# Performance work log

Measured on AMD Instinct MI355X. Metric: run time of the kernel, lower is better.

Reference implementation:

```python
import jax, jax.numpy as jnp
import numpy as np

EPS = 1e-5

def _layernorm(x, g, b):
    mu = jnp.mean(x, axis=-1, keepdims=True)
    var = jnp.mean((x - mu) ** 2, axis=-1, keepdims=True)
    return (x - mu) * jax.lax.rsqrt(var + EPS) * g + b

def setup_inputs() -> dict:
    key = jax.random.key(0)
    ks = jax.random.split(key, 16)
    B, C, H, W = 2, 64, 96, 96
    HID = 256
    s = 0.02
    inp = {
        "x": jax.random.normal(ks[0], (B, C, H, W), dtype=jnp.float32),
        "mask": jax.random.randint(ks[1], (B, H, W), 0, 2, dtype=jnp.int32),
        "wq": jax.random.normal(ks[2], (C, C), dtype=jnp.float32) * s,
        "bq": jnp.zeros((C,), dtype=jnp.float32),
        "wk": jax.random.normal(ks[3], (C, C), dtype=jnp.float32) * s,
        "bk": jnp.zeros((C,), dtype=jnp.float32),
        "wv": jax.random.normal(ks[4], (C, C), dtype=jnp.float32) * s,
        "bv": jnp.zeros((C,), dtype=jnp.float32),
        "wo": jax.random.normal(ks[5], (C, C), dtype=jnp.float32) * s,
        "bo": jnp.zeros((C,), dtype=jnp.float32),
        "g1": jnp.ones((C,), dtype=jnp.float32),
        "b1": jnp.zeros((C,), dtype=jnp.float32),
        "g2": jnp.ones((C,), dtype=jnp.float32),
        "b2": jnp.zeros((C,), dtype=jnp.float32),
        "w1": jax.random.normal(ks[6], (HID, C), dtype=jnp.float32) * s,
        "bf1": jnp.zeros((HID,), dtype=jnp.float32),
        "w2": jax.random.normal(ks[7], (C, HID), dtype=jnp.float32) * s,
        "bf2": jnp.zeros((C,), dtype=jnp.float32),
    }
    return inp

def reference(x, mask, wq, bq, wk, bk, wv, bv, wo, bo, g1, b1, g2, b2, w1, bf1, w2, bf2):
    B, C, H, W = x.shape
    scale = C ** (-0.5)
    xf = jnp.transpose(x, (0, 2, 3, 1)).reshape(B, H * W, C)   # [B,N,C]
    m = mask.reshape(B, H * W).astype(bool)                     # [B,N] valid pillars
    # pre-norm (original norms the gathered valid feats; LN is per-token so dense is equivalent)
    h = _layernorm(xf, g1, b1)
    q = h @ wq.T + bq
    k = h @ wk.T + bk
    v = h @ wv.T + bv
    scores = jnp.einsum('bnc,bmc->bnm', q, k) * scale
    scores = jnp.where(m[:, None, :], scores, -1e9)            # attend only among valid keys
    attn = jax.nn.softmax(scores, axis=-1)
    att = jnp.einsum('bnm,bmc->bnc', attn, v)
    h2 = h + (att @ wo.T + bo)                                  # residual onto norm1 output (as in source)
    h2 = _layernorm(h2, g2, b2)
    out = h2 + (jax.nn.gelu(h2 @ w1.T + bf1, approximate=False) @ w2.T + bf2)
    out = jnp.where(m[:, :, None], out, 0.0)                    # scatter-back: invalid positions are zeros
    return jnp.transpose(out.reshape(B, H, W, C), (0, 3, 1, 2))
```

## Files before the change

kernel.cpp:

```cpp
#include <hip/hip_runtime.h>

#define HW     9216
#define NTOK   18432
#define SPLITS 8
#define KIT    (HW / SPLITS / 32)

typedef float  floatx4 __attribute__((ext_vector_type(4)));
typedef short  short8  __attribute__((ext_vector_type(8)));
typedef short  short4v __attribute__((ext_vector_type(4)));
typedef int    int4v   __attribute__((ext_vector_type(4)));

#if __has_builtin(__builtin_amdgcn_exp2f)
#define EXP2F(x) __builtin_amdgcn_exp2f(x)
#else
#define EXP2F(x) exp2f(x)
#endif

__device__ __forceinline__ unsigned short f2bf(float f) {
  unsigned int u = __float_as_uint(f);
  u += 0x7fffu + ((u >> 16) & 1u);
  return (unsigned short)(u >> 16);
}
__device__ __forceinline__ float bf2f(unsigned short s) {
  return __uint_as_float(((unsigned int)s) << 16);
}
__device__ __forceinline__ int pk2(float a, float b) {
  unsigned ua = __float_as_uint(a) + 0x8000u;
  unsigned ub = __float_as_uint(b) + 0x8000u;
  return (int)((ua >> 16) | (ub & 0xffff0000u));
}

__global__ __launch_bounds__(256) void k_qkv(
    const float* __restrict__ x,
    const float* __restrict__ wq, const float* __restrict__ bq,
    const float* __restrict__ wk, const float* __restrict__ bk,
    const float* __restrict__ wv, const float* __restrict__ bv,
    const float* __restrict__ g1, const float* __restrict__ b1,
    const int* __restrict__ mask,
    const float* __restrict__ wo, const float* __restrict__ w1,
    const float* __restrict__ w2,
    unsigned short* __restrict__ h_bf, unsigned short* __restrict__ qg,
    unsigned short* __restrict__ ksw, unsigned short* __restrict__ vsw,
    float* __restrict__ maskf, unsigned short* __restrict__ wobf,
    unsigned short* __restrict__ w1bf, unsigned short* __restrict__ w2bf,
    float* __restrict__ cntb)
{
  __shared__ __align__(16) char usmem[27648];
  float (*xt)[33] = (float (*)[33])usmem;
  unsigned short (*wb)[64][72] = (unsigned short (*)[64][72])usmem;

  __shared__ unsigned short hq[32][72];
  __shared__ unsigned short kt[32][72];
  __shared__ unsigned short vt[64][40];
  __shared__ unsigned short qt[32][72];
  __shared__ float mk32[32];

  const int tid = threadIdx.x, wid = tid >> 6, c = tid & 63;
  const int mcol = c & 15, quad = c >> 4;
  const int bx = blockIdx.x;
  const int t0 = bx * 32;
  const int b  = t0 / HW, n0 = t0 % HW;

  if (tid < 32) {
    const float m = mask[t0 + tid] ? 1.f : 0.f;
    maskf[t0 + tid] = m;
    mk32[tid] = m;
  }
  if (wid == 0) {
    const bool mm = (c < 32) ? (mask[t0 + c] == 0) : false;
    const unsigned long long bal = __ballot(mm);
    if (c == 0) cntb[bx] = (float)__popcll(bal);
  }
  if (bx < 16)       { const int i = bx * 256 + tid;        wobf[i] = f2bf(wo[i]); }
  else if (bx < 80)  { const int i = (bx - 16) * 256 + tid; w1bf[i] = f2bf(w1[i]); }
  else if (bx < 144) { const int i = (bx - 80) * 256 + tid; w2bf[i] = f2bf(w2[i]); }

  #pragma unroll
  for (int p = 0; p < 2; ++p) {
    const int idx = p * 256 + tid;
    const int cc = idx >> 3, t4 = (idx & 7) * 4;
    const floatx4 v = *(const floatx4*)(x + ((long)b * 64 + cc) * HW + n0 + t4);
    xt[cc][t4 + 0] = v[0]; xt[cc][t4 + 1] = v[1];
    xt[cc][t4 + 2] = v[2]; xt[cc][t4 + 3] = v[3];
  }
  __syncthreads();

  {
    const float g1v = g1[c], b1v = b1[c];
    #pragma unroll
    for (int tt = 0; tt < 8; ++tt) {
      const int tok = wid * 8 + tt;
      const float val = xt[c][tok];
      float s = val, q = val * val;
      #pragma unroll
      for (int d = 1; d < 64; d <<= 1) { s += __shfl_xor(s, d); q += __shfl_xor(q, d); }
      const float mu  = s * (1.f / 64.f);
      const float var = q * (1.f / 64.f) - mu * mu;
      const float hv  = (val - mu) * rsqrtf(var + 1e-5f) * g1v + b1v;
      hq[tok][c] = f2bf(hv);
    }
  }
  __syncthreads();

  {
    const int tok = tid >> 3, c8 = (tid & 7) * 8;
    *(short8*)(h_bf + (long)(t0 + tok) * 64 + c8) = *(const short8*)(&hq[tok][c8]);
  }

  {
    auto conv = [&](const float* __restrict__ W, int mwi) {
      #pragma unroll
      for (int j = 0; j < 4; ++j) {
        const int idx4 = (j * 256 + tid) * 4;
        const int o = idx4 >> 6, in4 = idx4 & 63;
        const floatx4 w4 = *(const floatx4*)(W + idx4);
        short4v s4;
        s4[0] = (short)f2bf(w4[0]); s4[1] = (short)f2bf(w4[1]);
        s4[2] = (short)f2bf(w4[2]); s4[3] = (short)f2bf(w4[3]);
        *(short4v*)(&wb[mwi][o][in4]) = s4;
      }
    };
    conv(wq, 0); conv(wk, 1); conv(wv, 2);
  }
  __syncthreads();

  {
    const float QSC = 0.125f * 1.44269504088896f;
    #pragma unroll
    for (int i = 0; i < 6; ++i) {
      const int t = wid * 6 + i;
      const int mat  = t >> 3;
      const int tokT = (t >> 2) & 1;
      const int outT = t & 3;
      const int out  = outT * 16 + mcol;
      const short8 A0 = *(const short8*)(&hq[tokT * 16 + mcol][quad * 8]);
      const short8 A1 = *(const short8*)(&hq[tokT * 16 + mcol][32 + quad * 8]);
      const short8 B0 = *(const short8*)(&wb[mat][out][quad * 8]);
      const short8 B1 = *(const short8*)(&wb[mat][out][32 + quad * 8]);
      floatx4 d = (floatx4){0.f, 0.f, 0.f, 0.f};
      d = __builtin_amdgcn_mfma_f32_16x16x32_bf16(A0, B0, d, 0, 0, 0);
      d = __builtin_amdgcn_mfma_f32_16x16x32_bf16(A1, B1, d, 0, 0, 0);
      if (mat == 0) {
        const float bias = bq[out];
        #pragma unroll
        for (int r = 0; r < 4; ++r) {
          const int tok = tokT * 16 + quad * 4 + r;
          qt[tok][out] = f2bf((d[r] + bias) * QSC);
        }
      } else if (mat == 1) {
        const float bias = bk[out];
        #pragma unroll
        for (int r = 0; r < 4; ++r) {
          const int tok = tokT * 16 + quad * 4 + r;
          kt[tok][out] = f2bf((d[r] + bias) * mk32[tok]);
        }
      } else {
        const float bias = bv[out];
        #pragma unroll
        for (int r = 0; r < 4; ++r) {
          const int tok = tokT * 16 + quad * 4 + r;
          vt[out][tok] = f2bf((d[r] + bias) * mk32[tok]);
        }
      }
    }
  }
  __syncthreads();

  {
    const int tok = tid >> 3, c8 = (tid & 7) * 8;
    *(short8*)(qg + (long)(t0 + tok) * 64 + c8) = *(const short8*)(&qt[tok][c8]);
  }

  const long tile = (long)b * 288 + (n0 >> 5);
  {
    const int slot = tid >> 6, l = tid & 63;
    const int m = l & 15, qd = l >> 4, sub = slot >> 1, ss = slot & 1;
    const short8 v8 = *(const short8*)(&kt[sub * 16 + m][ss * 32 + qd * 8]);
    *(short8*)(ksw + tile * 2048 + tid * 8) = v8;
  }
  {
    const int f = tid >> 6, l = tid & 63;
    const int m = l & 15, qd = l >> 4;
    const short4v lo = *(const short4v*)(&vt[f * 16 + m][qd * 4]);
    const short4v hi = *(const short4v*)(&vt[f * 16 + m][16 + qd * 4]);
    short8 v8;
    v8[0] = lo[0]; v8[1] = lo[1]; v8[2] = lo[2]; v8[3] = lo[3];
    v8[4] = hi[0]; v8[5] = hi[1]; v8[6] = hi[2]; v8[7] = hi[3];
    *(short8*)(vsw + tile * 2048 + tid * 8) = v8;
  }
}

__global__ __launch_bounds__(256, 4) void k_attn(
    const unsigned short* __restrict__ qg, const unsigned short* __restrict__ ksw,
    const unsigned short* __restrict__ vsw,
    unsigned short* __restrict__ opart, float* __restrict__ lpart)
{
  __shared__ __align__(16) char smem[17408];

  const int tid = threadIdx.x, wid = tid >> 6, lane = tid & 63;
  const int mcol = lane & 15, quad = lane >> 4;
  const int bx = blockIdx.x;
  const int split = bx & (SPLITS - 1), qidx = bx / SPLITS;
  const int b = qidx / 48, qt = qidx % 48;
  const long t0q = (long)b * HW + qt * 192 + wid * 48;

  const unsigned short* kswt = ksw + ((long)b * 288 + split * KIT) * 2048;
  const unsigned short* vswt = vsw + ((long)b * 288 + split * KIT) * 2048;

  short8 qf[3][2];
  #pragma unroll
  for (int g = 0; g < 3; ++g)
    #pragma unroll
    for (int s = 0; s < 2; ++s)
      qf[g][s] = *(const short8*)(qg + (t0q + g * 16 + mcol) * 64 + s * 32 + quad * 8);

  short8 ones8;
  #pragma unroll
  for (int i = 0; i < 8; ++i) ones8[i] = (short)0x3F80;

  floatx4 oT[3][4], oL[3];
  #pragma unroll
  for (int g = 0; g < 3; ++g) {
    #pragma unroll
    for (int f = 0; f < 4; ++f) oT[g][f] = (floatx4){0.f,0.f,0.f,0.f};
    oL[g] = (floatx4){0.f,0.f,0.f,0.f};
  }

  short8 kr = *(const short8*)(kswt + tid * 8);
  short8 vr = *(const short8*)(vswt + tid * 8);
  *(short8*)((unsigned short*)smem + tid * 8) = kr;
  *(short8*)((unsigned short*)(smem + 4096) + tid * 8) = vr;
  __syncthreads();

  for (int it = 0; it < KIT; ++it) {
    const int off = (it & 1) * 8192;
    const unsigned short* kfc = (const unsigned short*)(smem + off);
    const unsigned short* vfc = (const unsigned short*)(smem + off + 4096);
    if (it + 1 < KIT) {
      kr = *(const short8*)(kswt + (it + 1) * 2048 + tid * 8);
      vr = *(const short8*)(vswt + (it + 1) * 2048 + tid * 8);
    }

    const short8 kA00 = *(const short8*)(kfc + (0 * 64 + lane) * 8);
    const short8 kA01 = *(const short8*)(kfc + (1 * 64 + lane) * 8);
    const short8 kA10 = *(const short8*)(kfc + (2 * 64 + lane) * 8);
    const short8 kA11 = *(const short8*)(kfc + (3 * 64 + lane) * 8);

    short8 pf[3];
    #pragma unroll
    for (int g = 0; g < 3; ++g) {
      floatx4 s0 = (floatx4){0.f,0.f,0.f,0.f}, s1 = (floatx4){0.f,0.f,0.f,0.f};
      s0 = __builtin_amdgcn_mfma_f32_16x16x32_bf16(kA00, qf[g][0], s0, 0, 0, 0);
      s0 = __builtin_amdgcn_mfma_f32_16x16x32_bf16(kA01, qf[g][1], s0, 0, 0, 0);
      s1 = __builtin_amdgcn_mfma_f32_16x16x32_bf16(kA10, qf[g][0], s1, 0, 0, 0);
      s1 = __builtin_amdgcn_mfma_f32_16x16x32_bf16(kA11, qf[g][1], s1, 0, 0, 0);

      int4v pv;
      pv[0] = pk2(EXP2F(s0[0]), EXP2F(s0[1]));
      pv[1] = pk2(EXP2F(s0[2]), EXP2F(s0[3]));
      pv[2] = pk2(EXP2F(s1[0]), EXP2F(s1[1]));
      pv[3] = pk2(EXP2F(s1[2]), EXP2F(s1[3]));
      pf[g] = __builtin_bit_cast(short8, pv);
      oL[g] = __builtin_amdgcn_mfma_f32_16x16x32_bf16(ones8, pf[g], oL[g], 0, 0, 0);
    }

    #pragma unroll
    for (int f = 0; f < 4; ++f) {
      const short8 vA = *(const short8*)(vfc + (f * 64 + lane) * 8);
      #pragma unroll
      for (int g = 0; g < 3; ++g)
        oT[g][f] = __builtin_amdgcn_mfma_f32_16x16x32_bf16(vA, pf[g], oT[g][f], 0, 0, 0);
    }

    if (it + 1 < KIT) {
      unsigned short* kfn = (unsigned short*)(smem + (off ^ 8192));
      unsigned short* vfn = (unsigned short*)(smem + (off ^ 8192) + 4096);
      *(short8*)(kfn + tid * 8) = kr;
      *(short8*)(vfn + tid * 8) = vr;
    }
    __syncthreads();
  }

  float* scr = (float*)smem + wid * 1088;
  #pragma unroll
  for (int g = 0; g < 3; ++g) {
    #pragma unroll
    for (int f = 0; f < 4; ++f)
      #pragma unroll
      for (int r = 0; r < 4; ++r)
        scr[(quad * 4 + r) * 68 + f * 16 + mcol] = oT[g][f][r];
    #pragma unroll
    for (int ps = 0; ps < 2; ++ps) {
      const int row = ps * 8 + (lane >> 3), cb = (lane & 7) * 8;
      const floatx4 a = *(const floatx4*)(scr + row * 68 + cb);
      const floatx4 c = *(const floatx4*)(scr + row * 68 + cb + 4);
      int4v pk;
      pk[0] = pk2(a[0], a[1]); pk[1] = pk2(a[2], a[3]);
      pk[2] = pk2(c[0], c[1]); pk[3] = pk2(c[2], c[3]);
      *(int4v*)(opart + ((long)split * NTOK + t0q + g * 16 + row) * 64 + cb) = pk;
    }
  }
  if (lane < 16) {
    #pragma unroll
    for (int g = 0; g < 3; ++g)
      lpart[(long)split * NTOK + t0q + g * 16 + lane] = oL[g][0];
  }
}

__global__ __launch_bounds__(256) void k_post(
    const unsigned short* __restrict__ opart, const float* __restrict__ lpart,
    const unsigned short* __restrict__ h_bf, const float* __restrict__ maskf,
    const float* __restrict__ cntb,
    const unsigned short* __restrict__ wobf, const float* __restrict__ bo,
    const float* __restrict__ g2, const float* __restrict__ b2,
    const unsigned short* __restrict__ w1bf, const float* __restrict__ bf1,
    const unsigned short* __restrict__ w2bf, const float* __restrict__ bf2,
    float* __restrict__ out)
{
  __shared__ float          h2_lds[32 * 68];
  __shared__ unsigned short att_lds[32 * 72];
  __shared__ unsigned short hn_lds[32 * 72];
  __shared__ unsigned short g_lds[32 * 264];
  __shared__ float          ot_lds[32 * 68];
  __shared__ float          linv[32];
  __shared__ float          st_mu[32], st_rs[32];
  __shared__ float          nred[4];

  const int tid = threadIdx.x, wid = tid >> 6, lane = tid & 63;
  const int mcol = lane & 15, quad = lane >> 4;
  const int t0 = blockIdx.x * 32;
  const int b = t0 / HW, n0 = t0 % HW;

  {
    float cacc = 0.f;
    for (int i = tid; i < 288; i += 256) cacc += cntb[b * 288 + i];
    #pragma unroll
    for (int d = 1; d < 64; d <<= 1) cacc += __shfl_xor(cacc, d);
    if (lane == 0) nred[wid] = cacc;
  }

  const int tok = tid >> 3, c8 = (tid & 7) * 8;
  float o[8];
  #pragma unroll
  for (int i = 0; i < 8; ++i) o[i] = 0.f;
  #pragma unroll
  for (int s = 0; s < SPLITS; ++s) {
    const short8 op = *(const short8*)(opart + ((long)s * NTOK + t0 + tok) * 64 + c8);
    #pragma unroll
    for (int i = 0; i < 8; ++i) o[i] += bf2f((unsigned short)op[i]);
  }
  const short8 hb8 = *(const short8*)(h_bf + (long)(t0 + tok) * 64 + c8);
  const floatx4 bo0 = *(const floatx4*)(bo + c8);
  const floatx4 bo1 = *(const floatx4*)(bo + c8 + 4);
  __syncthreads();

  if (tid < 32) {
    float l = -((nred[0] + nred[1]) + (nred[2] + nred[3]));
    #pragma unroll
    for (int s = 0; s < SPLITS; ++s) l += lpart[(long)s * NTOK + t0 + tid];
    linv[tid] = 1.0f / l;
  }
  __syncthreads();
  {
    const float sc = linv[tok];
    int4v av;
    av[0] = pk2(o[0]*sc, o[1]*sc); av[1] = pk2(o[2]*sc, o[3]*sc);
    av[2] = pk2(o[4]*sc, o[5]*sc); av[3] = pk2(o[6]*sc, o[7]*sc);
    *(int4v*)(att_lds + tok * 72 + c8) = av;
    floatx4 h20, h21;
    #pragma unroll
    for (int i = 0; i < 4; ++i) {
      h20[i] = bf2f((unsigned short)hb8[i])     + bo0[i];
      h21[i] = bf2f((unsigned short)hb8[i + 4]) + bo1[i];
    }
    *(floatx4*)(h2_lds + tok * 68 + c8)     = h20;
    *(floatx4*)(h2_lds + tok * 68 + c8 + 4) = h21;
  }
  __syncthreads();

  const int Mt = wid & 1, nbase = (wid >> 1) * 2;
  {
    const short8 aA0 = *(const short8*)(att_lds + (Mt * 16 + mcol) * 72 + quad * 8);
    const short8 aA1 = *(const short8*)(att_lds + (Mt * 16 + mcol) * 72 + 32 + quad * 8);
    #pragma unroll
    for (int nt = 0; nt < 2; ++nt) {
      const int nc = (nbase + nt) * 16;
      const short8 b0 = *(const short8*)(wobf + (nc + mcol) * 64 + quad * 8);
      const short8 b1 = *(const short8*)(wobf + (nc + mcol) * 64 + 32 + quad * 8);
      floatx4 d = (floatx4){0.f,0.f,0.f,0.f};
      d = __builtin_amdgcn_mfma_f32_16x16x32_bf16(aA0, b0, d, 0, 0, 0);
      d = __builtin_amdgcn_mfma_f32_16x16x32_bf16(aA1, b1, d, 0, 0, 0);
      #pragma unroll
      for (int r = 0; r < 4; ++r)
        h2_lds[(Mt * 16 + quad * 4 + r) * 68 + nc + mcol] += d[r];
    }
  }
  __syncthreads();

  {
    floatx4 v0 = *(const floatx4*)(h2_lds + tok * 68 + c8);
    floatx4 v1 = *(const floatx4*)(h2_lds + tok * 68 + c8 + 4);
    float s1 = (v0[0]+v0[1])+(v0[2]+v0[3]) + (v1[0]+v1[1])+(v1[2]+v1[3]);
    float s2 = (v0[0]*v0[0]+v0[1]*v0[1])+(v0[2]*v0[2]+v0[3]*v0[3])
             + (v1[0]*v1[0]+v1[1]*v1[1])+(v1[2]*v1[2]+v1[3]*v1[3]);
    #pragma unroll
    for (int d = 1; d < 8; d <<= 1) { s1 += __shfl_xor(s1, d); s2 += __shfl_xor(s2, d); }
    if ((tid & 7) == 0) {
      const float mu = s1 * (1.f / 64.f);
      const float var = s2 * (1.f / 64.f) - mu * mu;
      st_mu[tok] = mu; st_rs[tok] = rsqrtf(var + 1e-5f);
    }
  }
  __syncthreads();

  {
    const float mu = st_mu[tok], rs = st_rs[tok];
    const floatx4 v0 = *(const floatx4*)(h2_lds + tok * 68 + c8);
    const floatx4 v1 = *(const floatx4*)(h2_lds + tok * 68 + c8 + 4);
    const floatx4 ga = *(const floatx4*)(g2 + c8), gb = *(const floatx4*)(g2 + c8 + 4);
    const floatx4 ba = *(const floatx4*)(b2 + c8), bb = *(const floatx4*)(b2 + c8 + 4);
    float hn[8];
    #pragma unroll
    for (int i = 0; i < 4; ++i) {
      hn[i]     = (v0[i] - mu) * rs * ga[i] + ba[i];
      hn[i + 4] = (v1[i] - mu) * rs * gb[i] + bb[i];
    }
    int4v hv;
    hv[0] = pk2(hn[0], hn[1]); hv[1] = pk2(hn[2], hn[3]);
    hv[2] = pk2(hn[4], hn[5]); hv[3] = pk2(hn[6], hn[7]);
    *(int4v*)(hn_lds + tok * 72 + c8) = hv;
  }
  __syncthreads();

  {
    const short8 aA0 = *(const short8*)(hn_lds + (Mt * 16 + mcol) * 72 + quad * 8);
    const short8 aA1 = *(const short8*)(hn_lds + (Mt * 16 + mcol) * 72 + 32 + quad * 8);
    #pragma unroll
    for (int nt = 0; nt < 8; ++nt) {
      const int u0 = ((wid >> 1) * 8 + nt) * 16;
      const short8 b0 = *(const short8*)(w1bf + (u0 + mcol) * 64 + quad * 8);
      const short8 b1 = *(const short8*)(w1bf + (u0 + mcol) * 64 + 32 + quad * 8);
      floatx4 d = (floatx4){0.f,0.f,0.f,0.f};
      d = __builtin_amdgcn_mfma_f32_16x16x32_bf16(aA0, b0, d, 0, 0, 0);
      d = __builtin_amdgcn_mfma_f32_16x16x32_bf16(aA1, b1, d, 0, 0, 0);
      const float bf1v = bf1[u0 + mcol];
      #pragma unroll
      for (int r = 0; r < 4; ++r) {
        const float a = d[r] + bf1v;
        const float gl = 0.5f * a * (1.0f + erff(a * 0.70710678118654752f));
        g_lds[(Mt * 16 + quad * 4 + r) * 264 + u0 + mcol] = f2bf(gl);
      }
    }
  }
  __syncthreads();

  {
    floatx4 acc[2];
    acc[0] = (floatx4){0.f,0.f,0.f,0.f}; acc[1] = (floatx4){0.f,0.f,0.f,0.f};
    #pragma unroll
    for (int ks = 0; ks < 8; ++ks) {
      const short8 aA = *(const short8*)(g_lds + (Mt * 16 + mcol) * 264 + ks * 32 + quad * 8);
      #pragma unroll
      for (int nt = 0; nt < 2; ++nt) {
        const int nc = (nbase + nt) * 16;
        const short8 bB = *(const short8*)(w2bf + (nc + mcol) * 256 + ks * 32 + quad * 8);
        acc[nt] = __builtin_amdgcn_mfma_f32_16x16x32_bf16(aA, bB, acc[nt], 0, 0, 0);
      }
    }
    #pragma unroll
    for (int nt = 0; nt < 2; ++nt) {
      const int cc = (nbase + nt) * 16 + mcol;
      const float g2v = g2[cc], b2v = b2[cc], bf2v = bf2[cc];
      #pragma unroll
      for (int r = 0; r < 4; ++r) {
        const int tokr = Mt * 16 + quad * 4 + r;
        const float hn = (h2_lds[tokr * 68 + cc] - st_mu[tokr]) * st_rs[tokr] * g2v + b2v;
        const float o2 = (hn + acc[nt][r] + bf2v) * maskf[t0 + tokr];
        ot_lds[tokr * 68 + cc] = o2;
      }
    }
  }
  __syncthreads();

  {
    const int c = tid >> 2, tg = (tid & 3) * 8;
    floatx4 v0, v1;
    #pragma unroll
    for (int i = 0; i < 4; ++i) {
      v0[i] = ot_lds[(tg + i) * 68 + c];
      v1[i] = ot_lds[(tg + 4 + i) * 68 + c];
    }
    float* dst = out + ((long)b * 64 + c) * HW + n0 + tg;
    *(floatx4*)dst = v0;
    *(floatx4*)(dst + 4) = v1;
  }
}

extern "C" void kernel_launch(void* const* d_in, const int* in_sizes, int n_in,
                              void* d_out, int out_size, void* d_ws, size_t ws_size,
                              hipStream_t stream) {
  (void)in_sizes; (void)n_in; (void)out_size; (void)ws_size;
  const float* x   = (const float*)d_in[0];
  const int*   msk = (const int*)  d_in[1];
  const float* wq  = (const float*)d_in[2];
  const float* bq  = (const float*)d_in[3];
  const float* wk  = (const float*)d_in[4];
  const float* bk  = (const float*)d_in[5];
  const float* wv  = (const float*)d_in[6];
  const float* bv  = (const float*)d_in[7];
  const float* wo  = (const float*)d_in[8];
  const float* bo  = (const float*)d_in[9];
  const float* g1  = (const float*)d_in[10];
  const float* b1  = (const float*)d_in[11];
  const float* g2  = (const float*)d_in[12];
  const float* b2  = (const float*)d_in[13];
  const float* w1  = (const float*)d_in[14];
  const float* bf1 = (const float*)d_in[15];
  const float* w2  = (const float*)d_in[16];
  const float* bf2 = (const float*)d_in[17];
  float* out = (float*)d_out;

  char* ws = (char*)d_ws;
  size_t off = 0;
  unsigned short* h_bf  = (unsigned short*)(ws + off); off += 2359296;
  unsigned short* qg    = (unsigned short*)(ws + off); off += 2359296;
  unsigned short* ksw   = (unsigned short*)(ws + off); off += 2359296;
  unsigned short* vsw   = (unsigned short*)(ws + off); off += 2359296;
  unsigned short* opart = (unsigned short*)(ws + off); off += (size_t)SPLITS * NTOK * 64 * 2;
  float*          lpart = (float*)(ws + off);          off += (size_t)SPLITS * NTOK * 4;
  float*          maskf = (float*)(ws + off);          off += 73728;
  unsigned short* wobf  = (unsigned short*)(ws + off); off += 8192;
  unsigned short* w1bf  = (unsigned short*)(ws + off); off += 32768;
  unsigned short* w2bf  = (unsigned short*)(ws + off); off += 32768;
  float*          cntb  = (float*)(ws + off);          off += 2304;

  k_qkv<<<dim3(576), dim3(256), 0, stream>>>(
      x, wq, bq, wk, bk, wv, bv, g1, b1, msk, wo, w1, w2,
      h_bf, qg, ksw, vsw, maskf, wobf, w1bf, w2bf, cntb);
  k_attn<<<dim3(96 * SPLITS), dim3(256), 0, stream>>>(qg, ksw, vsw, opart, lpart);
  k_post<<<dim3(576), dim3(256), 0, stream>>>(
      opart, lpart, h_bf, maskf, cntb, wobf, bo, g2, b2, w1bf, bf1, w2bf, bf2, out);
}
```

Baseline: 160.7 us.

## Load K/V fragments directly from global into registers, drop LDS staging and barriers

The attention loop no longer stages K and V tiles through shared memory with a double buffer and a __syncthreads per iteration. Each wave now reads its pre-swizzled MFMA fragments straight from global memory, prefetching the next K tile into a ping-pong register set while V is loaded per iteration. This removes LDS traffic and block-wide barriers. In exchange each of the four waves in a block loads the same K/V data from global/L2, so global traffic per block rises by about four times, and the extra registers lower the launch-bounds occupancy hint from 4 to 3.

```diff
diff --git a/kernel.cpp b/kernel.cpp
--- a/kernel.cpp
+++ b/kernel.cpp
@@ -190,7 +190,7 @@
   }
 }
 
-__global__ __launch_bounds__(256, 4) void k_attn(
+__global__ __launch_bounds__(256, 3) void k_attn(
     const unsigned short* __restrict__ qg, const unsigned short* __restrict__ ksw,
     const unsigned short* __restrict__ vsw,
     unsigned short* __restrict__ opart, float* __restrict__ lpart)
@@ -226,60 +226,51 @@
     oL[g] = (floatx4){0.f,0.f,0.f,0.f};
   }
 
-  short8 kr = *(const short8*)(kswt + tid * 8);
-  short8 vr = *(const short8*)(vswt + tid * 8);
-  *(short8*)((unsigned short*)smem + tid * 8) = kr;
-  *(short8*)((unsigned short*)(smem + 4096) + tid * 8) = vr;
-  __syncthreads();
-
-  for (int it = 0; it < KIT; ++it) {
-    const int off = (it & 1) * 8192;
-    const unsigned short* kfc = (const unsigned short*)(smem + off);
-    const unsigned short* vfc = (const unsigned short*)(smem + off + 4096);
-    if (it + 1 < KIT) {
-      kr = *(const short8*)(kswt + (it + 1) * 2048 + tid * 8);
-      vr = *(const short8*)(vswt + (it + 1) * 2048 + tid * 8);
-    }
-
-    const short8 kA00 = *(const short8*)(kfc + (0 * 64 + lane) * 8);
-    const short8 kA01 = *(const short8*)(kfc + (1 * 64 + lane) * 8);
-    const short8 kA10 = *(const short8*)(kfc + (2 * 64 + lane) * 8);
-    const short8 kA11 = *(const short8*)(kfc + (3 * 64 + lane) * 8);
-
-    short8 pf[3];
-    #pragma unroll
-    for (int g = 0; g < 3; ++g) {
-      floatx4 s0 = (floatx4){0.f,0.f,0.f,0.f}, s1 = (floatx4){0.f,0.f,0.f,0.f};
-      s0 = __builtin_amdgcn_mfma_f32_16x16x32_bf16(kA00, qf[g][0], s0, 0, 0, 0);
-      s0 = __builtin_amdgcn_mfma_f32_16x16x32_bf16(kA01, qf[g][1], s0, 0, 0, 0);
-      s1 = __builtin_amdgcn_mfma_f32_16x16x32_bf16(kA10, qf[g][0], s1, 0, 0, 0);
-      s1 = __builtin_amdgcn_mfma_f32_16x16x32_bf16(kA11, qf[g][1], s1, 0, 0, 0);
-
-      int4v pv;
-      pv[0] = pk2(EXP2F(s0[0]), EXP2F(s0[1]));
-      pv[1] = pk2(EXP2F(s0[2]), EXP2F(s0[3]));
-      pv[2] = pk2(EXP2F(s1[0]), EXP2F(s1[1]));
-      pv[3] = pk2(EXP2F(s1[2]), EXP2F(s1[3]));
-      pf[g] = __builtin_bit_cast(short8, pv);
-      oL[g] = __builtin_amdgcn_mfma_f32_16x16x32_bf16(ones8, pf[g], oL[g], 0, 0, 0);
-    }
-
-    #pragma unroll
-    for (int f = 0; f < 4; ++f) {
-      const short8 vA = *(const short8*)(vfc + (f * 64 + lane) * 8);
-      #pragma unroll
-      for (int g = 0; g < 3; ++g)
-        oT[g][f] = __builtin_amdgcn_mfma_f32_16x16x32_bf16(vA, pf[g], oT[g][f], 0, 0, 0);
-    }
-
-    if (it + 1 < KIT) {
-      unsigned short* kfn = (unsigned short*)(smem + (off ^ 8192));
-      unsigned short* vfn = (unsigned short*)(smem + (off ^ 8192) + 4096);
-      *(short8*)(kfn + tid * 8) = kr;
-      *(short8*)(vfn + tid * 8) = vr;
-    }
-    __syncthreads();
-  }
+  short8 ka[4], kb[4];
+  #pragma unroll
+  for (int s = 0; s < 4; ++s)
+    ka[s] = *(const short8*)(kswt + (s * 64 + lane) * 8);
+
+#define ATTN_ITER(IT, KCUR, KNXT)                                              \
+  {                                                                            \
+    short8 cv[4];                                                              \
+    _Pragma("unroll")                                                          \
+    for (int f = 0; f < 4; ++f)                                                \
+      cv[f] = *(const short8*)(vswt + (IT) * 2048 + (f * 64 + lane) * 8);      \
+    if ((IT) + 1 < KIT) {                                                      \
+      _Pragma("unroll")                                                        \
+      for (int s = 0; s < 4; ++s)                                              \
+        KNXT[s] = *(const short8*)(kswt + ((IT) + 1) * 2048 + (s * 64 + lane) * 8); \
+    }                                                                          \
+    short8 pf[3];                                                              \
+    _Pragma("unroll")                                                          \
+    for (int g = 0; g < 3; ++g) {                                              \
+      floatx4 s0 = (floatx4){0.f,0.f,0.f,0.f}, s1 = (floatx4){0.f,0.f,0.f,0.f};\
+      s0 = __builtin_amdgcn_mfma_f32_16x16x32_bf16(KCUR[0], qf[g][0], s0, 0, 0, 0); \
+      s0 = __builtin_amdgcn_mfma_f32_16x16x32_bf16(KCUR[1], qf[g][1], s0, 0, 0, 0); \
+      s1 = __builtin_amdgcn_mfma_f32_16x16x32_bf16(KCUR[2], qf[g][0], s1, 0, 0, 0); \
+      s1 = __builtin_amdgcn_mfma_f32_16x16x32_bf16(KCUR[3], qf[g][1], s1, 0, 0, 0); \
+      int4v pv;                                                                \
+      pv[0] = pk2(EXP2F(s0[0]), EXP2F(s0[1]));                                 \
+      pv[1] = pk2(EXP2F(s0[2]), EXP2F(s0[3]));                                 \
+      pv[2] = pk2(EXP2F(s1[0]), EXP2F(s1[1]));                                 \
+      pv[3] = pk2(EXP2F(s1[2]), EXP2F(s1[3]));                                 \
+      pf[g] = __builtin_bit_cast(short8, pv);                                  \
+      oL[g] = __builtin_amdgcn_mfma_f32_16x16x32_bf16(ones8, pf[g], oL[g], 0, 0, 0); \
+    }                                                                          \
+    _Pragma("unroll")                                                          \
+    for (int f = 0; f < 4; ++f) {                                              \
+      _Pragma("unroll")                                                        \
+      for (int g = 0; g < 3; ++g)                                              \
+        oT[g][f] = __builtin_amdgcn_mfma_f32_16x16x32_bf16(cv[f], pf[g], oT[g][f], 0, 0, 0); \
+    }                                                                          \
+  }
+
+  for (int it = 0; it < KIT; it += 2) {
+    ATTN_ITER(it,     ka, kb);
+    ATTN_ITER(it + 1, kb, ka);
+  }
+#undef ATTN_ITER
 
   float* scr = (float*)smem + wid * 1088;
   #pragma unroll
```

Result: no change. 159.9 us (-0.5%).
